# Kernel optimization log

Hardware: AMD Instinct MI355X
Metric: run time of the kernel (lower is better)

Reference implementation:

```python
import jax, jax.numpy as jnp
import numpy as np

ORDER = 2


def _masked_row_mean(v, m, safe_cnt, has_any):
    # v already zeroed outside mask; per-row mean over masked entries
    s = jnp.sum(v, axis=1, keepdims=True) / safe_cnt
    return jnp.where(has_any, s, 0.0)


def high_order_residual(x, mask, order=ORDER):
    """Vectorized faithful version of high_order_residual (braq).
    nanmean over masked entries == masked sum / count; sign/scale/shift
    are only meaningful inside the mask, outputs outside the mask are 0.
    """
    m = mask.astype(x.dtype)                       # (oc, ic)
    cnt = jnp.sum(m, axis=1, keepdims=True)        # (oc, 1)
    safe_cnt = jnp.maximum(cnt, 1.0)
    has_any = cnt > 0
    xm = x * m
    sum_order = jnp.zeros_like(x)
    for _ in range(order):
        residual = (xm - sum_order) * m            # masked residual, 0 outside
        mean = _masked_row_mean(residual, m, safe_cnt, has_any)   # (oc,1)
        centered = (residual - mean) * m           # 0 outside mask
        scale = _masked_row_mean(jnp.abs(centered), m, safe_cnt, has_any)
        binary = jnp.sign(centered) * scale + mean
        sum_order = sum_order + binary * m
    return sum_order


def setup_inputs() -> dict:
    key = jax.random.key(0)
    k1, k2 = jax.random.split(key)
    x = jax.random.normal(k1, (11008, 4096), dtype=jnp.float32) * 0.02
    mask = jax.random.randint(k2, (11008, 4096), 0, 2).astype(jnp.bool_)
    return {"x": x, "mask": mask}


def reference(x, mask):
    return high_order_residual(x, mask, ORDER)
```

## Files before the change

kernel.cpp:

```cpp
#include <hip/hip_runtime.h>
#include <stdint.h>

#define IC    4096
#define BLK   512
#define VPT   2
#define EPT   8
#define RPB   4

__device__ __forceinline__ void bred_df(double& a, float& p, double* smd, float* smf) {
    #pragma unroll
    for (int off = 32; off; off >>= 1) { a += __shfl_xor(a, off); p += __shfl_xor(p, off); }
    const int wid = threadIdx.x >> 6;
    if ((threadIdx.x & 63) == 0) { smd[wid] = a; smf[wid] = p; }
    __syncthreads();
    a = ((smd[0]+smd[1])+(smd[2]+smd[3])) + ((smd[4]+smd[5])+(smd[6]+smd[7]));
    p = ((smf[0]+smf[1])+(smf[2]+smf[3])) + ((smf[4]+smf[5])+(smf[6]+smf[7]));
}

__device__ __forceinline__ double bred_d(double a, double* smd) {
    #pragma unroll
    for (int off = 32; off; off >>= 1) a += __shfl_xor(a, off);
    const int wid = threadIdx.x >> 6;
    if ((threadIdx.x & 63) == 0) smd[wid] = a;
    __syncthreads();
    return ((smd[0]+smd[1])+(smd[2]+smd[3])) + ((smd[4]+smd[5])+(smd[6]+smd[7]));
}

__device__ __forceinline__ uint32_t byte4_to_bits(uint32_t w) {
    return (uint32_t)((w & 0x000000ffu) != 0)
         | ((uint32_t)((w & 0x0000ff00u) != 0) << 1)
         | ((uint32_t)((w & 0x00ff0000u) != 0) << 2)
         | ((uint32_t)((w & 0xff000000u) != 0) << 3);
}

__device__ __forceinline__ void row_compute(
    const float (&xin)[EPT], uint32_t mb, float4* orow4,
    int tid, double* smd, float* smf)
{
    float xm[EPT];
    float sgm[EPT];

    #pragma unroll
    for (int j = 0; j < EPT; ++j) xm[j] = ((mb >> j) & 1u) ? xin[j] : 0.f;

    double s0 = 0.0, s1 = 0.0;
    #pragma unroll
    for (int j = 0; j < EPT; j += 2) { s0 += (double)xm[j]; s1 += (double)xm[j+1]; }
    double s  = s0 + s1;
    float  cf = (float)__popc(mb);
    bred_df(s, cf, smd + 0, smf + 0);

    const bool   has    = (cf > 0.f);
    const double c      = (double)cf;
    const double nmiss  = (double)(4096.f - cf);
    const double inv    = 1.0 / fmax(c, 1.0);
    const double mean1  = has ? s * inv : 0.0;
    const float  mean1f = (float)mean1;

    double sa0 = 0.0, sa1 = 0.0;
    float  d0 = 0.f, d1 = 0.f;
    #pragma unroll
    for (int j = 0; j < EPT; ++j) {
        const float t  = xm[j] - mean1f;
        const float sg = (t > 0.f) ? 1.f : ((t < 0.f) ? -1.f : 0.f);
        const float sv = ((mb >> j) & 1u) ? sg : 0.f;
        sgm[j] = sv;
        if (j & 1) { d1 += sv; sa1 += (double)fabsf(t); }
        else       { d0 += sv; sa0 += (double)fabsf(t); }
    }
    double sa = sa0 + sa1;
    float  df = d0 + d1;
    bred_df(sa, df, smd + 8, smf + 8);
    sa -= nmiss * (double)fabsf(mean1f);

    const double scale1 = has ? sa * inv : 0.0;
    const double mean2  = has ? (s - scale1 * (double)df - mean1 * c) * inv : 0.0;
    const double mean12 = mean1 + mean2;

    double sb0 = 0.0, sb1 = 0.0;
    #pragma unroll
    for (int j = 0; j < EPT; ++j) {
        const double t2 = (double)xm[j] - fma((double)sgm[j], scale1, mean12);
        sgm[j] = (float)t2;
        if (j & 1) sb1 += fabs(t2); else sb0 += fabs(t2);
    }
    double sa2 = bred_d(sb0 + sb1, smd + 16);
    sa2 -= nmiss * fabs(mean12);
    const double scale2  = has ? sa2 * inv : 0.0;
    const float  scale2f = (float)scale2;

    #pragma unroll
    for (int i = 0; i < VPT; ++i) {
        float r[4];
        #pragma unroll
        for (int k = 0; k < 4; ++k) {
            const int j = 4 * i + k;
            const float t2f = sgm[j];
            const float b1f = xm[j] - t2f;
            const float sg2 = (t2f > 0.f) ? 1.f : ((t2f < 0.f) ? -1.f : 0.f);
            r[k] = ((mb >> j) & 1u) ? fmaf(sg2, scale2f, b1f) : 0.f;
        }
        float4 o; o.x = r[0]; o.y = r[1]; o.z = r[2]; o.w = r[3];
        orow4[tid + i * BLK] = o;
    }
}

__global__ __launch_bounds__(BLK, 8) void binarize_kernel(
    const float* __restrict__ x,
    const uint8_t* __restrict__ mask,
    float* __restrict__ out,
    int nrows)
{
    __shared__ double smd[24];
    __shared__ float  smf[16];
    const int tid   = threadIdx.x;
    const int lane  = tid & 63;
    const int rbase = (int)blockIdx.x * RPB;

    const bool mask_is_i32 = !__any(((const uint32_t*)mask)[lane] > 1u);

    if (!mask_is_i32) {
        float4   nxa, nxb;
        uint32_t nma, nmb;
        {
            const int r = rbase;
            const float4*   xr = (const float4*)(x + (size_t)r * IC);
            const uint32_t* mr = (const uint32_t*)(mask + (size_t)r * IC);
            nxa = xr[tid];       nxb = xr[tid + BLK];
            nma = mr[tid];       nmb = mr[tid + BLK];
        }
        #pragma unroll
        for (int k = 0; k < RPB; ++k) {
            const int r = rbase + k;
            if (r >= nrows) break;
            float xin[EPT];
            xin[0] = nxa.x; xin[1] = nxa.y; xin[2] = nxa.z; xin[3] = nxa.w;
            xin[4] = nxb.x; xin[5] = nxb.y; xin[6] = nxb.z; xin[7] = nxb.w;
            const uint32_t mb = byte4_to_bits(nma) | (byte4_to_bits(nmb) << 4);

            const int rn = rbase + k + 1;
            if (k + 1 < RPB && rn < nrows) {
                const float4*   xr = (const float4*)(x + (size_t)rn * IC);
                const uint32_t* mr = (const uint32_t*)(mask + (size_t)rn * IC);
                nxa = xr[tid];   nxb = xr[tid + BLK];
                nma = mr[tid];   nmb = mr[tid + BLK];
            }
            row_compute(xin, mb, (float4*)(out + (size_t)r * IC), tid, smd, smf);
        }
    } else {
        for (int k = 0; k < RPB; ++k) {
            const int r = rbase + k;
            if (r >= nrows) break;
            const float4* xr = (const float4*)(x + (size_t)r * IC);
            const int4*   mr = (const int4*)mask + (size_t)r * (IC / 4);
            float xin[EPT]; uint32_t mb = 0;
            #pragma unroll
            for (int i = 0; i < VPT; ++i) {
                const float4 v  = xr[tid + i * BLK];
                const int4   m4 = mr[tid + i * BLK];
                xin[4*i+0] = v.x; xin[4*i+1] = v.y; xin[4*i+2] = v.z; xin[4*i+3] = v.w;
                mb |= ((uint32_t)(m4.x != 0) | ((uint32_t)(m4.y != 0) << 1)
                    |  ((uint32_t)(m4.z != 0) << 2) | ((uint32_t)(m4.w != 0) << 3)) << (4 * i);
            }
            row_compute(xin, mb, (float4*)(out + (size_t)r * IC), tid, smd, smf);
        }
    }
}

extern "C" void kernel_launch(void* const* d_in, const int* in_sizes, int n_in,
                              void* d_out, int out_size, void* d_ws, size_t ws_size,
                              hipStream_t stream) {
    const float*   x    = (const float*)d_in[0];
    const uint8_t* mask = (const uint8_t*)d_in[1];
    float*         out  = (float*)d_out;

    const int rows = in_sizes[0] / IC;
    const int grid = (rows + RPB - 1) / RPB;
    binarize_kernel<<<grid, BLK, 0, stream>>>(x, mask, out, rows);
}
```

Before: 424.1 us.

## Halve block size, double elements per thread, recompute signs instead of storing

Each row is now handled by 256 threads with 16 elements per thread, so block reductions span 4 waves instead of 8. The per-element sign/residual array is dropped and recomputed in later passes to save registers. The prefetch of the first row is hoisted before the mask-type check, and the occupancy hint is lowered to 6. This aims to shorten reduction and sync cost per row and to keep more loads in flight, at the cost of extra ALU work and higher per-thread register use. The first-row prefetch also runs unconditionally in the int32-mask branch, where it reads the mask with a different stride, which is wasted work there.

```diff
diff --git a/kernel.cpp b/kernel.cpp
--- a/kernel.cpp
+++ b/kernel.cpp
@@ -1,11 +1,11 @@
 #include <hip/hip_runtime.h>
 #include <stdint.h>
 
-#define IC    4096
-#define BLK   512
-#define VPT   2
-#define EPT   8
-#define RPB   4
+#define IC   4096
+#define BLK  256
+#define VPT  4
+#define EPT  16
+#define RPB  4
 
 __device__ __forceinline__ void bred_df(double& a, float& p, double* smd, float* smf) {
     #pragma unroll
@@ -13,8 +13,8 @@
     const int wid = threadIdx.x >> 6;
     if ((threadIdx.x & 63) == 0) { smd[wid] = a; smf[wid] = p; }
     __syncthreads();
-    a = ((smd[0]+smd[1])+(smd[2]+smd[3])) + ((smd[4]+smd[5])+(smd[6]+smd[7]));
-    p = ((smf[0]+smf[1])+(smf[2]+smf[3])) + ((smf[4]+smf[5])+(smf[6]+smf[7]));
+    a = (smd[0] + smd[1]) + (smd[2] + smd[3]);
+    p = (smf[0] + smf[1]) + (smf[2] + smf[3]);
 }
 
 __device__ __forceinline__ double bred_d(double a, double* smd) {
@@ -23,7 +23,7 @@
     const int wid = threadIdx.x >> 6;
     if ((threadIdx.x & 63) == 0) smd[wid] = a;
     __syncthreads();
-    return ((smd[0]+smd[1])+(smd[2]+smd[3])) + ((smd[4]+smd[5])+(smd[6]+smd[7]));
+    return (smd[0] + smd[1]) + (smd[2] + smd[3]);
 }
 
 __device__ __forceinline__ uint32_t byte4_to_bits(uint32_t w) {
@@ -38,8 +38,6 @@
     int tid, double* smd, float* smf)
 {
     float xm[EPT];
-    float sgm[EPT];
-
     #pragma unroll
     for (int j = 0; j < EPT; ++j) xm[j] = ((mb >> j) & 1u) ? xin[j] : 0.f;
 
@@ -64,13 +62,12 @@
         const float t  = xm[j] - mean1f;
         const float sg = (t > 0.f) ? 1.f : ((t < 0.f) ? -1.f : 0.f);
         const float sv = ((mb >> j) & 1u) ? sg : 0.f;
-        sgm[j] = sv;
         if (j & 1) { d1 += sv; sa1 += (double)fabsf(t); }
         else       { d0 += sv; sa0 += (double)fabsf(t); }
     }
     double sa = sa0 + sa1;
     float  df = d0 + d1;
-    bred_df(sa, df, smd + 8, smf + 8);
+    bred_df(sa, df, smd + 4, smf + 4);
     sa -= nmiss * (double)fabsf(mean1f);
 
     const double scale1 = has ? sa * inv : 0.0;
@@ -80,11 +77,13 @@
     double sb0 = 0.0, sb1 = 0.0;
     #pragma unroll
     for (int j = 0; j < EPT; ++j) {
-        const double t2 = (double)xm[j] - fma((double)sgm[j], scale1, mean12);
-        sgm[j] = (float)t2;
+        const float t   = xm[j] - mean1f;
+        const float sg  = (t > 0.f) ? 1.f : ((t < 0.f) ? -1.f : 0.f);
+        const float sv  = ((mb >> j) & 1u) ? sg : 0.f;
+        const double t2 = (double)xm[j] - fma((double)sv, scale1, mean12);
         if (j & 1) sb1 += fabs(t2); else sb0 += fabs(t2);
     }
-    double sa2 = bred_d(sb0 + sb1, smd + 16);
+    double sa2 = bred_d(sb0 + sb1, smd + 8);
     sa2 -= nmiss * fabs(mean12);
     const double scale2  = has ? sa2 * inv : 0.0;
     const float  scale2f = (float)scale2;
@@ -95,7 +94,11 @@
         #pragma unroll
         for (int k = 0; k < 4; ++k) {
             const int j = 4 * i + k;
-            const float t2f = sgm[j];
+            const float t   = xm[j] - mean1f;
+            const float sg  = (t > 0.f) ? 1.f : ((t < 0.f) ? -1.f : 0.f);
+            const float sv  = ((mb >> j) & 1u) ? sg : 0.f;
+            const double t2 = (double)xm[j] - fma((double)sv, scale1, mean12);
+            const float t2f = (float)t2;
             const float b1f = xm[j] - t2f;
             const float sg2 = (t2f > 0.f) ? 1.f : ((t2f < 0.f) ? -1.f : 0.f);
             r[k] = ((mb >> j) & 1u) ? fmaf(sg2, scale2f, b1f) : 0.f;
@@ -105,45 +108,43 @@
     }
 }
 
-__global__ __launch_bounds__(BLK, 8) void binarize_kernel(
+__global__ __launch_bounds__(BLK, 6) void binarize_kernel(
     const float* __restrict__ x,
     const uint8_t* __restrict__ mask,
     float* __restrict__ out,
     int nrows)
 {
-    __shared__ double smd[24];
-    __shared__ float  smf[16];
+    __shared__ double smd[12];
+    __shared__ float  smf[8];
     const int tid   = threadIdx.x;
     const int lane  = tid & 63;
     const int rbase = (int)blockIdx.x * RPB;
 
+    const float4*   x4r  = (const float4*)x + (size_t)rbase * (IC / 4);
+    const uint32_t* m32r = (const uint32_t*)mask + (size_t)rbase * (IC / 4);
+
+    float4   fx0 = x4r[tid], fx1 = x4r[tid + BLK], fx2 = x4r[tid + 2*BLK], fx3 = x4r[tid + 3*BLK];
+    uint32_t fm0 = m32r[tid], fm1 = m32r[tid + BLK], fm2 = m32r[tid + 2*BLK], fm3 = m32r[tid + 3*BLK];
     const bool mask_is_i32 = !__any(((const uint32_t*)mask)[lane] > 1u);
 
     if (!mask_is_i32) {
-        float4   nxa, nxb;
-        uint32_t nma, nmb;
-        {
-            const int r = rbase;
-            const float4*   xr = (const float4*)(x + (size_t)r * IC);
-            const uint32_t* mr = (const uint32_t*)(mask + (size_t)r * IC);
-            nxa = xr[tid];       nxb = xr[tid + BLK];
-            nma = mr[tid];       nmb = mr[tid + BLK];
-        }
         #pragma unroll
         for (int k = 0; k < RPB; ++k) {
             const int r = rbase + k;
             if (r >= nrows) break;
             float xin[EPT];
-            xin[0] = nxa.x; xin[1] = nxa.y; xin[2] = nxa.z; xin[3] = nxa.w;
-            xin[4] = nxb.x; xin[5] = nxb.y; xin[6] = nxb.z; xin[7] = nxb.w;
-            const uint32_t mb = byte4_to_bits(nma) | (byte4_to_bits(nmb) << 4);
+            xin[ 0]=fx0.x; xin[ 1]=fx0.y; xin[ 2]=fx0.z; xin[ 3]=fx0.w;
+            xin[ 4]=fx1.x; xin[ 5]=fx1.y; xin[ 6]=fx1.z; xin[ 7]=fx1.w;
+            xin[ 8]=fx2.x; xin[ 9]=fx2.y; xin[10]=fx2.z; xin[11]=fx2.w;
+            xin[12]=fx3.x; xin[13]=fx3.y; xin[14]=fx3.z; xin[15]=fx3.w;
+            const uint32_t mb = byte4_to_bits(fm0)        | (byte4_to_bits(fm1) << 4)
+                              | (byte4_to_bits(fm2) << 8) | (byte4_to_bits(fm3) << 12);
 
-            const int rn = rbase + k + 1;
-            if (k + 1 < RPB && rn < nrows) {
-                const float4*   xr = (const float4*)(x + (size_t)rn * IC);
-                const uint32_t* mr = (const uint32_t*)(mask + (size_t)rn * IC);
-                nxa = xr[tid];   nxb = xr[tid + BLK];
-                nma = mr[tid];   nmb = mr[tid + BLK];
+            if (k + 1 < RPB && r + 1 < nrows) {
+                const float4*   xn = (const float4*)x + (size_t)(r + 1) * (IC / 4);
+                const uint32_t* mn = (const uint32_t*)mask + (size_t)(r + 1) * (IC / 4);
+                fx0 = xn[tid]; fx1 = xn[tid + BLK]; fx2 = xn[tid + 2*BLK]; fx3 = xn[tid + 3*BLK];
+                fm0 = mn[tid]; fm1 = mn[tid + BLK]; fm2 = mn[tid + 2*BLK]; fm3 = mn[tid + 3*BLK];
             }
             row_compute(xin, mb, (float4*)(out + (size_t)r * IC), tid, smd, smf);
         }
@@ -151,7 +152,7 @@
         for (int k = 0; k < RPB; ++k) {
             const int r = rbase + k;
             if (r >= nrows) break;
-            const float4* xr = (const float4*)(x + (size_t)r * IC);
+            const float4* xr = (const float4*)x + (size_t)r * (IC / 4);
             const int4*   mr = (const int4*)mask + (size_t)r * (IC / 4);
             float xin[EPT]; uint32_t mb = 0;
             #pragma unroll
```

Measured after the change: 420.4 us. Within noise of the previous version (-0.9%).
